# Kernel optimization log

Hardware: AMD Instinct MI355X
Metric: run time of the kernel (lower is better)

The kernel has to match this reference:

```python
import jax, jax.numpy as jnp
import numpy as np

C, H, W, D, M = 64, 512, 512, 4, 16


def setup_inputs() -> dict:
    key = jax.random.key(0)
    ks = jax.random.split(key, 9)
    scale = (1.0 / (C * C)) ** 0.5
    return {
        "q": jax.random.normal(ks[0], (1, 1, H, W), jnp.float32),
        "proj_w": jax.random.normal(ks[1], (C, 1, 1, 1), jnp.float32),
        "proj_b": jax.random.normal(ks[2], (C, 1, 1), jnp.float32) * 0.01,
        "spec_wr": jax.random.normal(ks[3], (D, C, C, M, M), jnp.float32) * scale,
        "spec_wi": jax.random.normal(ks[4], (D, C, C, M, M), jnp.float32) * scale,
        "w_w": jax.random.normal(ks[5], (D, C, C, 1, 1), jnp.float32) * (1.0 / C ** 0.5),
        "w_b": jax.random.normal(ks[6], (D, C, 1, 1), jnp.float32) * 0.01,
        "final_w": jax.random.normal(ks[7], (1, C, 1, 1), jnp.float32) * (1.0 / C ** 0.5),
        "final_b": jax.random.normal(ks[8], (1, 1, 1), jnp.float32) * 0.01,
    }


def _spectral(x, wr, wi, m):
    # x: (C,H,W). FFT2 -> contract low modes -> zero-pad -> iFFT2, take real part.
    Cin, Hh, Ww = x.shape
    x_ft = jnp.fft.fft2(x, axes=(-2, -1))  # (C,H,W) complex
    w = (wr + 1j * wi).astype(x_ft.dtype)  # (Cin,Cout,m,m)
    out_sub = jnp.einsum('imn,iomn->omn', x_ft[:, :m, :m], w)
    out_ft = jnp.zeros((wr.shape[1], Hh, Ww), dtype=x_ft.dtype).at[:, :m, :m].set(out_sub)
    return jnp.fft.ifft2(out_ft, axes=(-2, -1)).real


def reference(q, proj_w, proj_b, spec_wr, spec_wi, w_w, w_b, final_w, final_b):
    m = spec_wr.shape[-1]
    depth = spec_wr.shape[0]
    x = q[0].astype(jnp.float32)  # (C_in,H,W) -- batch must be 1
    # 1x1 conv lift
    x = jnp.einsum('oi,ihw->ohw', proj_w[:, :, 0, 0], x) + proj_b
    for d in range(depth):
        x_spec = _spectral(x, spec_wr[d], spec_wi[d], m)
        x_local = jnp.einsum('oi,ihw->ohw', w_w[d, :, :, 0, 0], x) + w_b[d]
        x = jax.nn.gelu(x_spec + x_local)
    x = jnp.einsum('oi,ihw->ohw', final_w[:, :, 0, 0], x) + final_b
    return x[None]  # re-add batch dim
```

## Files before the change

### kernel.cpp

```cpp
#include <hip/hip_runtime.h>
#include <cmath>

#define CC 64
#define HH 512
#define WWID 512
#define HWSZ (HH*WWID)
#define DEPTH 4

typedef __attribute__((ext_vector_type(8))) short short8;
typedef __attribute__((ext_vector_type(4))) float floatx4;

__device__ inline unsigned short f2bf(float f){
  unsigned int u = __float_as_uint(f);
  u += 0x7FFF + ((u >> 16) & 1);
  return (unsigned short)(u >> 16);
}
__device__ inline float bf2f(unsigned short h){
  return __uint_as_float(((unsigned int)h) << 16);
}

__global__ void k_init(const float* __restrict__ ww,
                       float* __restrict__ ctab, float* __restrict__ stab,
                       unsigned short* __restrict__ trigBh, unsigned short* __restrict__ trigBl,
                       unsigned short* __restrict__ trigTh, unsigned short* __restrict__ trigTl,
                       unsigned short* __restrict__ Whi, unsigned short* __restrict__ Wlo,
                       float4* __restrict__ Xfz){
  if (blockIdx.x < 32) Xfz[blockIdx.x*256 + threadIdx.x] = make_float4(0.f,0.f,0.f,0.f);
  int idx = blockIdx.x*256 + threadIdx.x;
  if (idx < 8192){
    int pos = idx >> 4, k = idx & 15;
    int r = (pos * k) & 511;
    double ang = (2.0 * 3.14159265358979323846 / 512.0) * (double)r;
    float c = (float)cos(ang), s = (float)sin(ang);
    ctab[idx] = c;  stab[idx] = s;
    unsigned short ch = f2bf(c), sh = f2bf(s);
    unsigned short cl = f2bf(c - bf2f(ch)), sl = f2bf(s - bf2f(sh));
    trigBh[pos*32 + 2*k]     = ch;  trigBl[pos*32 + 2*k]     = cl;
    trigBh[pos*32 + 2*k + 1] = sh;  trigBl[pos*32 + 2*k + 1] = sl;
    trigTh[(2*k)*512 + pos]   = ch;  trigTl[(2*k)*512 + pos]   = cl;
    trigTh[(2*k+1)*512 + pos] = sh;  trigTl[(2*k+1)*512 + pos] = sl;
  } else {
    int t = idx - 8192;
    float v = ww[t];
    unsigned short h = f2bf(v);
    Whi[t] = h;  Wlo[t] = f2bf(v - bf2f(h));
  }
}

#define APITCH 136
#define XPITCH 33
template<int LIFT>
__global__ __launch_bounds__(256) void k_dftw(const unsigned int* __restrict__ xp,
    const float* __restrict__ qsrc, const float* __restrict__ pw, const float* __restrict__ pb,
    const unsigned short* __restrict__ trigTh, const unsigned short* __restrict__ trigTl,
    const float* __restrict__ ctab, const float* __restrict__ stab,
    float* __restrict__ Xfa, float4* __restrict__ Yz){
  if (blockIdx.x < 32) Yz[blockIdx.x*256 + threadIdx.x] = make_float4(0.f,0.f,0.f,0.f);

  __shared__ unsigned short Ahs[64*APITCH], Als[64*APITCH];
  __shared__ unsigned short Bhs[32*APITCH], Bls[32*APITCH];
  __shared__ float X1s[64*XPITCH];
  int row0 = blockIdx.x * 64;
  int i  = row0 >> 9;
  int h0 = row0 & 511;
  int t = threadIdx.x;
  int g = t >> 6, lm = t & 15, lq = (t >> 4) & 3;
  float pa = 0.f, pbv = 0.f;
  if (LIFT){ pa = pw[i]; pbv = pb[i]; }

  floatx4 acc[2] = {{0.f,0.f,0.f,0.f},{0.f,0.f,0.f,0.f}};

  for (int kc = 0; kc < 4; ++kc){
    {
      int r = t >> 2, qq = t & 3;
      unsigned int* dh = (unsigned int*)&Ahs[r*APITCH + qq*32];
      unsigned int* dl = (unsigned int*)&Als[r*APITCH + qq*32];
      if (LIFT){
        const float4* src4 = (const float4*)(qsrc + (size_t)(h0 + r)*512 + kc*128 + qq*32);
        #pragma unroll
        for (int u = 0; u < 8; ++u){
          float4 v = src4[u];
          v.x = fmaf(pa, v.x, pbv); v.y = fmaf(pa, v.y, pbv);
          v.z = fmaf(pa, v.z, pbv); v.w = fmaf(pa, v.w, pbv);
          unsigned short h0_ = f2bf(v.x), h1 = f2bf(v.y), h2 = f2bf(v.z), h3 = f2bf(v.w);
          unsigned short g0 = f2bf(v.x - bf2f(h0_)), g1 = f2bf(v.y - bf2f(h1));
          unsigned short g2 = f2bf(v.z - bf2f(h2)), g3 = f2bf(v.w - bf2f(h3));
          uint2 ph, pl;
          ph.x = (unsigned)h0_ | ((unsigned)h1 << 16);
          ph.y = (unsigned)h2 | ((unsigned)h3 << 16);
          pl.x = (unsigned)g0 | ((unsigned)g1 << 16);
          pl.y = (unsigned)g2 | ((unsigned)g3 << 16);
          *(uint2*)&dh[u*2] = ph;
          *(uint2*)&dl[u*2] = pl;
        }
      } else {
        const uint4* srcp = (const uint4*)(xp + ((size_t)(h0 + r)*64 + i)*512 + kc*128 + qq*32);
        #pragma unroll
        for (int u = 0; u < 8; ++u){
          uint4 v = srcp[u];
          uint2 ph, pl;
          ph.x = (v.x & 0xffffu) | (v.y << 16);
          ph.y = (v.z & 0xffffu) | (v.w << 16);
          pl.x = (v.x >> 16) | (v.y & 0xffff0000u);
          pl.y = (v.z >> 16) | (v.w & 0xffff0000u);
          *(uint2*)&dh[u*2] = ph;
          *(uint2*)&dl[u*2] = pl;
        }
      }
    }
    {
      int j = t >> 3, qq = t & 7;
      const uint4* sh = (const uint4*)((const unsigned int*)trigTh + j*256 + kc*64 + qq*8);
      const uint4* sl = (const uint4*)((const unsigned int*)trigTl + j*256 + kc*64 + qq*8);
      uint4* dh = (uint4*)&Bhs[j*APITCH + qq*16];
      uint4* dl = (uint4*)&Bls[j*APITCH + qq*16];
      dh[0] = sh[0]; dh[1] = sh[1];
      dl[0] = sl[0]; dl[1] = sl[1];
    }
    __syncthreads();
    #pragma unroll
    for (int ks = 0; ks < 4; ++ks){
      short8 ah = *(const short8*)&Ahs[(g*16 + lm)*APITCH + ks*32 + lq*8];
      short8 al = *(const short8*)&Als[(g*16 + lm)*APITCH + ks*32 + lq*8];
      #pragma unroll
      for (int nt = 0; nt < 2; ++nt){
        short8 bh = *(const short8*)&Bhs[(nt*16 + lm)*APITCH + ks*32 + lq*8];
        short8 bl = *(const short8*)&Bls[(nt*16 + lm)*APITCH + ks*32 + lq*8];
        acc[nt] = __builtin_amdgcn_mfma_f32_16x16x32_bf16(ah, bh, acc[nt], 0, 0, 0);
        acc[nt] = __builtin_amdgcn_mfma_f32_16x16x32_bf16(ah, bl, acc[nt], 0, 0, 0);
        acc[nt] = __builtin_amdgcn_mfma_f32_16x16x32_bf16(al, bh, acc[nt], 0, 0, 0);
      }
    }
    __syncthreads();
  }
  #pragma unroll
  for (int nt = 0; nt < 2; ++nt){
    int j = nt*16 + lm;
    float sgn = (j & 1) ? -1.f : 1.f;
    #pragma unroll
    for (int rg = 0; rg < 4; ++rg){
      int m = g*16 + lq*4 + rg;
      X1s[m*XPITCH + j] = sgn * acc[nt][rg];
    }
  }
  __syncthreads();

  int mo = t >> 4, n = t & 15;
  float ar = 0.f, ai = 0.f;
  #pragma unroll 8
  for (int hh = 0; hh < 64; ++hh){
    int h = h0 + hh;
    float Re = X1s[hh*XPITCH + 2*n];
    float Im = X1s[hh*XPITCH + 2*n + 1];
    float c = ctab[h*16 + mo], s = stab[h*16 + mo];
    ar += Re*c + Im*s;
    ai += Im*c - Re*s;
  }
  atomicAdd(&Xfa[(i*256 + t)*2],     ar);
  atomicAdd(&Xfa[(i*256 + t)*2 + 1], ai);
}

__global__ void k_contract(const float2* __restrict__ Xf,
                           const float* __restrict__ wr, const float* __restrict__ wi,
                           float* __restrict__ Ya){
  int o = blockIdx.x, ic = blockIdx.y;
  int mn = blockIdx.z*64 + threadIdx.x;
  float ar = 0.f, ai = 0.f;
  int i0 = ic * 16;
  #pragma unroll
  for (int ii = 0; ii < 16; ++ii){
    int i = i0 + ii;
    float2 xf = Xf[i*256 + mn];
    float wrv = wr[(i*64 + o)*256 + mn];
    float wiv = wi[(i*64 + o)*256 + mn];
    ar += xf.x*wrv - xf.y*wiv;
    ai += xf.x*wiv + xf.y*wrv;
  }
  const float sc = 1.f/262144.f;
  atomicAdd(&Ya[(o*256 + mn)*2],     ar*sc);
  atomicAdd(&Ya[(o*256 + mn)*2 + 1], ai*sc);
}

__global__ void k_idfth(const float2* __restrict__ Y, const float* __restrict__ ct,
                        const float* __restrict__ st,
                        unsigned int* __restrict__ Thi, unsigned int* __restrict__ Tlo,
                        float4* __restrict__ Xfz){
  if (blockIdx.x < 32) Xfz[blockIdx.x*256 + threadIdx.x] = make_float4(0.f,0.f,0.f,0.f);
  int idx = blockIdx.x*256 + threadIdx.x;
  int n = idx & 15, o = (idx >> 4) & 63, h = idx >> 10;
  float ar = 0.f, ai = 0.f;
  #pragma unroll
  for (int m = 0; m < 16; ++m){
    float2 y = Y[(o<<8) + (m<<4) + n];
    float c = ct[h*16 + m], s = st[h*16 + m];
    ar += y.x*c - y.y*s;
    ai += y.x*s + y.y*c;
  }
  float tr = ar, ts = -ai;
  unsigned short rh = f2bf(tr), sh = f2bf(ts);
  Thi[idx] = (unsigned int)rh | ((unsigned int)sh << 16);
  unsigned short rl = f2bf(tr - bf2f(rh)), slr = f2bf(ts - bf2f(sh));
  Tlo[idx] = (unsigned int)rl | ((unsigned int)slr << 16);
}

#define PITCH 104
template<int LIFT, int FINAL>
__global__ __launch_bounds__(256) void k_combine(
    const unsigned int* __restrict__ xp, const float* __restrict__ qsrc,
    const float* __restrict__ pw, const float* __restrict__ pb,
    const unsigned short* __restrict__ Whid, const unsigned short* __restrict__ Wlod,
    const unsigned int* __restrict__ Thi,  const unsigned int* __restrict__ Tlo,
    const unsigned short* __restrict__ trigBh, const unsigned short* __restrict__ trigBl,
    const float* __restrict__ wb, unsigned int* __restrict__ xo,
    const float* __restrict__ fw, const float* __restrict__ fb,
    float* __restrict__ outp)
{
  __shared__ unsigned short Ah[64*PITCH],  Al[64*PITCH];
  __shared__ unsigned short Bh[128*PITCH], Bl[128*PITCH];
  int h  = blockIdx.y;
  int w0 = blockIdx.x * 128;
  int t  = threadIdx.x;

  {
    int wl = t & 127, ig = t >> 7;
    if (LIFT){
      float qv = qsrc[(size_t)h*512 + w0 + wl];
      #pragma unroll
      for (int ii = 0; ii < 32; ii += 4){
        int i0 = ig*32 + ii;
        float v0 = fmaf(pw[i0],   qv, pb[i0]);
        float v1 = fmaf(pw[i0+1], qv, pb[i0+1]);
        float v2 = fmaf(pw[i0+2], qv, pb[i0+2]);
        float v3 = fmaf(pw[i0+3], qv, pb[i0+3]);
        unsigned short h0 = f2bf(v0), h1 = f2bf(v1), h2 = f2bf(v2), h3 = f2bf(v3);
        unsigned short g0 = f2bf(v0 - bf2f(h0)), g1 = f2bf(v1 - bf2f(h1));
        unsigned short g2 = f2bf(v2 - bf2f(h2)), g3 = f2bf(v3 - bf2f(h3));
        uint2 ph, pl;
        ph.x = (unsigned)h0 | ((unsigned)h1 << 16);
        ph.y = (unsigned)h2 | ((unsigned)h3 << 16);
        pl.x = (unsigned)g0 | ((unsigned)g1 << 16);
        pl.y = (unsigned)g2 | ((unsigned)g3 << 16);
        *(uint2*)&Bh[wl*PITCH + i0] = ph;
        *(uint2*)&Bl[wl*PITCH + i0] = pl;
      }
    } else {
      const unsigned int* xb = xp + (size_t)h*32768 + w0 + wl;
      #pragma unroll
      for (int ii = 0; ii < 32; ii += 4){
        int i0 = ig*32 + ii;
        unsigned int v0 = xb[(size_t)(i0  )*512];
        unsigned int v1 = xb[(size_t)(i0+1)*512];
        unsigned int v2 = xb[(size_t)(i0+2)*512];
        unsigned int v3 = xb[(size_t)(i0+3)*512];
        uint2 ph, pl;
        ph.x = (v0 & 0xffffu) | (v1 << 16);
        ph.y = (v2 & 0xffffu) | (v3 << 16);
        pl.x = (v0 >> 16) | (v1 & 0xffff0000u);
        pl.y = (v2 >> 16) | (v3 & 0xffff0000u);
        *(uint2*)&Bh[wl*PITCH + i0] = ph;
        *(uint2*)&Bl[wl*PITCH + i0] = pl;
      }
    }
  }
  {
    int row = t >> 1, qq = t & 1;
    const uint4* sh = (const uint4*)((const unsigned int*)trigBh + (size_t)(w0+row)*16 + qq*8);
    const uint4* sl = (const uint4*)((const unsigned int*)trigBl + (size_t)(w0+row)*16 + qq*8);
    uint4* dh = (uint4*)((unsigned int*)&Bh[row*PITCH + 64] + qq*8);
    uint4* dl = (uint4*)((unsigned int*)&Bl[row*PITCH + 64] + qq*8);
    dh[0] = sh[0]; dh[1] = sh[1];
    dl[0] = sl[0]; dl[1] = sl[1];
  }
  {
    int o = t >> 2, q8 = t & 3;
    const uint4* sh = (const uint4*)((const unsigned int*)Whid + o*32 + q8*8);
    const uint4* sl = (const uint4*)((const unsigned int*)Wlod + o*32 + q8*8);
    uint4* dh = (uint4*)((unsigned int*)&Ah[o*PITCH] + q8*8);
    uint4* dl = (uint4*)((unsigned int*)&Al[o*PITCH] + q8*8);
    dh[0] = sh[0]; dh[1] = sh[1];
    dl[0] = sl[0]; dl[1] = sl[1];
  }
  {
    int o = t >> 2, q4 = t & 3;
    const uint4* sh = (const uint4*)(Thi + (size_t)h*1024 + o*16 + q4*4);
    const uint4* sl = (const uint4*)(Tlo + (size_t)h*1024 + o*16 + q4*4);
    uint4* dh = (uint4*)((unsigned int*)&Ah[o*PITCH + 64] + q4*4);
    uint4* dl = (uint4*)((unsigned int*)&Al[o*PITCH + 64] + q4*4);
    dh[0] = sh[0];
    dl[0] = sl[0];
  }
  __syncthreads();

  int g  = t >> 6;
  int lm = t & 15;
  int lq = (t >> 4) & 3;

  floatx4 acc[8] = {{0.f,0.f,0.f,0.f},{0.f,0.f,0.f,0.f},{0.f,0.f,0.f,0.f},{0.f,0.f,0.f,0.f},
                    {0.f,0.f,0.f,0.f},{0.f,0.f,0.f,0.f},{0.f,0.f,0.f,0.f},{0.f,0.f,0.f,0.f}};

  #pragma unroll
  for (int ks = 0; ks < 3; ++ks){
    short8 af = *(const short8*)&Ah[(g*16 + lm)*PITCH + ks*32 + lq*8];
    short8 al = *(const short8*)&Al[(g*16 + lm)*PITCH + ks*32 + lq*8];
    #pragma unroll
    for (int nt = 0; nt < 8; ++nt){
      short8 bf = *(const short8*)&Bh[(nt*16 + lm)*PITCH + ks*32 + lq*8];
      short8 bl = *(const short8*)&Bl[(nt*16 + lm)*PITCH + ks*32 + lq*8];
      acc[nt] = __builtin_amdgcn_mfma_f32_16x16x32_bf16(af, bf, acc[nt], 0, 0, 0);
      acc[nt] = __builtin_amdgcn_mfma_f32_16x16x32_bf16(af, bl, acc[nt], 0, 0, 0);
      acc[nt] = __builtin_amdgcn_mfma_f32_16x16x32_bf16(al, bf, acc[nt], 0, 0, 0);
    }
  }

  if (!FINAL){
    #pragma unroll
    for (int nt = 0; nt < 8; ++nt){
      int w = w0 + nt*16 + lm;
      #pragma unroll
      for (int rg = 0; rg < 4; ++rg){
        int o = g*16 + lq*4 + rg;
        float u = acc[nt][rg] + wb[o];
        float z = 0.7978845608028654f * fmaf(0.044715f, u*u*u, u);
        float e = __expf(2.f*z);
        float gl = u - __fdividef(u, e + 1.f);
        unsigned short hi_ = f2bf(gl);
        unsigned short lo_ = f2bf(gl - bf2f(hi_));
        xo[((size_t)h*64 + o)*512 + w] = (unsigned int)hi_ | ((unsigned int)lo_ << 16);
      }
    }
  } else {
    float* fred = (float*)Ah;
    __syncthreads();
    #pragma unroll
    for (int nt = 0; nt < 8; ++nt){
      float partial = 0.f;
      #pragma unroll
      for (int rg = 0; rg < 4; ++rg){
        int o = g*16 + lq*4 + rg;
        float u = acc[nt][rg] + wb[o];
        float z = 0.7978845608028654f * fmaf(0.044715f, u*u*u, u);
        float e = __expf(2.f*z);
        float gl = u - __fdividef(u, e + 1.f);
        partial = fmaf(fw[o], gl, partial);
      }
      fred[(nt*16 + lm)*17 + (t >> 4)] = partial;
    }
    __syncthreads();
    if (t < 128){
      float s = fb[0];
      #pragma unroll
      for (int k2 = 0; k2 < 16; ++k2) s += fred[t*17 + k2];
      outp[(size_t)h*512 + w0 + t] = s;
    }
  }
}

extern "C" void kernel_launch(void* const* d_in, const int* in_sizes, int n_in,
                              void* d_out, int out_size, void* d_ws, size_t ws_size,
                              hipStream_t stream) {
  const float* q       = (const float*)d_in[0];
  const float* proj_w  = (const float*)d_in[1];
  const float* proj_b  = (const float*)d_in[2];
  const float* spec_wr = (const float*)d_in[3];
  const float* spec_wi = (const float*)d_in[4];
  const float* w_w     = (const float*)d_in[5];
  const float* w_b     = (const float*)d_in[6];
  const float* final_w = (const float*)d_in[7];
  const float* final_b = (const float*)d_in[8];
  float* out = (float*)d_out;

  char* ws = (char*)d_ws;
  float*  ctab = (float*) (ws + 0);
  float*  stab = (float*) (ws + 32768);
  unsigned short* trigBh = (unsigned short*)(ws + 65536);
  unsigned short* trigBl = (unsigned short*)(ws + 98304);
  unsigned int* Thi = (unsigned int*)(ws + 131072);
  unsigned int* Tlo = (unsigned int*)(ws + 2228224);
  float*  Xf   = (float*) (ws + 4325376);
  float*  Y    = (float*) (ws + 4456448);
  unsigned int* x = (unsigned int*)(ws + 4587520);
  unsigned short* Whi = (unsigned short*)(ws + 71696384);
  unsigned short* Wlo = (unsigned short*)(ws + 71729152);
  unsigned short* trigTh = (unsigned short*)(ws + 71761920);
  unsigned short* trigTl = (unsigned short*)(ws + 71794688);

  k_init<<<96, 256, 0, stream>>>(w_w, ctab, stab, trigBh, trigBl, trigTh, trigTl,
                                 Whi, Wlo, (float4*)Xf);

  for (int d = 0; d < DEPTH; ++d){
    if (d == 0)
      k_dftw<1><<<512, 256, 0, stream>>>(x, q, proj_w, proj_b, trigTh, trigTl,
                                         ctab, stab, Xf, (float4*)Y);
    else
      k_dftw<0><<<512, 256, 0, stream>>>(x, q, proj_w, proj_b, trigTh, trigTl,
                                         ctab, stab, Xf, (float4*)Y);
    k_contract<<<dim3(64,4,4), 64, 0, stream>>>((const float2*)Xf,
                                                spec_wr + (size_t)d*1048576,
                                                spec_wi + (size_t)d*1048576, Y);
    k_idfth<<<2048, 256, 0, stream>>>((const float2*)Y, ctab, stab, Thi, Tlo,
                                      (float4*)Xf);
    if (d == 0)
      k_combine<1,0><<<dim3(4,512), 256, 0, stream>>>(x, q, proj_w, proj_b,
          Whi + d*4096, Wlo + d*4096, Thi, Tlo, trigBh, trigBl,
          w_b + d*64, x, final_w, final_b, out);
    else if (d < DEPTH-1)
      k_combine<0,0><<<dim3(4,512), 256, 0, stream>>>(x, q, proj_w, proj_b,
          Whi + d*4096, Wlo + d*4096, Thi, Tlo, trigBh, trigBl,
          w_b + d*64, x, final_w, final_b, out);
    else
      k_combine<0,1><<<dim3(4,512), 256, 0, stream>>>(x, q, proj_w, proj_b,
          Whi + d*4096, Wlo + d*4096, Thi, Tlo, trigBh, trigBl,
          w_b + d*64, x, final_w, final_b, out);
  }
}
```

Before: 326.5 us.

## Load combine-kernel B operands directly from global into registers, dropping LDS staging

```diff
diff --git a/kernel.cpp b/kernel.cpp
--- a/kernel.cpp
+++ b/kernel.cpp
@@ -205,7 +205,7 @@
 
 #define PITCH 104
 template<int LIFT, int FINAL>
-__global__ __launch_bounds__(256) void k_combine(
+__global__ __launch_bounds__(256, 4) void k_combine(
     const unsigned int* __restrict__ xp, const float* __restrict__ qsrc,
     const float* __restrict__ pw, const float* __restrict__ pb,
     const unsigned short* __restrict__ Whid, const unsigned short* __restrict__ Wlod,
@@ -215,62 +215,11 @@
     const float* __restrict__ fw, const float* __restrict__ fb,
     float* __restrict__ outp)
 {
-  __shared__ unsigned short Ah[64*PITCH],  Al[64*PITCH];
-  __shared__ unsigned short Bh[128*PITCH], Bl[128*PITCH];
+  __shared__ unsigned short Ah[64*PITCH], Al[64*PITCH];
   int h  = blockIdx.y;
   int w0 = blockIdx.x * 128;
   int t  = threadIdx.x;
 
-  {
-    int wl = t & 127, ig = t >> 7;
-    if (LIFT){
-      float qv = qsrc[(size_t)h*512 + w0 + wl];
-      #pragma unroll
-      for (int ii = 0; ii < 32; ii += 4){
-        int i0 = ig*32 + ii;
-        float v0 = fmaf(pw[i0],   qv, pb[i0]);
-        float v1 = fmaf(pw[i0+1], qv, pb[i0+1]);
-        float v2 = fmaf(pw[i0+2], qv, pb[i0+2]);
-        float v3 = fmaf(pw[i0+3], qv, pb[i0+3]);
-        unsigned short h0 = f2bf(v0), h1 = f2bf(v1), h2 = f2bf(v2), h3 = f2bf(v3);
-        unsigned short g0 = f2bf(v0 - bf2f(h0)), g1 = f2bf(v1 - bf2f(h1));
-        unsigned short g2 = f2bf(v2 - bf2f(h2)), g3 = f2bf(v3 - bf2f(h3));
-        uint2 ph, pl;
-        ph.x = (unsigned)h0 | ((unsigned)h1 << 16);
-        ph.y = (unsigned)h2 | ((unsigned)h3 << 16);
-        pl.x = (unsigned)g0 | ((unsigned)g1 << 16);
-        pl.y = (unsigned)g2 | ((unsigned)g3 << 16);
-        *(uint2*)&Bh[wl*PITCH + i0] = ph;
-        *(uint2*)&Bl[wl*PITCH + i0] = pl;
-      }
-    } else {
-      const unsigned int* xb = xp + (size_t)h*32768 + w0 + wl;
-      #pragma unroll
-      for (int ii = 0; ii < 32; ii += 4){
-        int i0 = ig*32 + ii;
-        unsigned int v0 = xb[(size_t)(i0  )*512];
-        unsigned int v1 = xb[(size_t)(i0+1)*512];
-        unsigned int v2 = xb[(size_t)(i0+2)*512];
-        unsigned int v3 = xb[(size_t)(i0+3)*512];
-        uint2 ph, pl;
-        ph.x = (v0 & 0xffffu) | (v1 << 16);
-        ph.y = (v2 & 0xffffu) | (v3 << 16);
-        pl.x = (v0 >> 16) | (v1 & 0xffff0000u);
-        pl.y = (v2 >> 16) | (v3 & 0xffff0000u);
-        *(uint2*)&Bh[wl*PITCH + i0] = ph;
-        *(uint2*)&Bl[wl*PITCH + i0] = pl;
-      }
-    }
-  }
-  {
-    int row = t >> 1, qq = t & 1;
-    const uint4* sh = (const uint4*)((const unsigned int*)trigBh + (size_t)(w0+row)*16 + qq*8);
-    const uint4* sl = (const uint4*)((const unsigned int*)trigBl + (size_t)(w0+row)*16 + qq*8);
-    uint4* dh = (uint4*)((unsigned int*)&Bh[row*PITCH + 64] + qq*8);
-    uint4* dl = (uint4*)((unsigned int*)&Bl[row*PITCH + 64] + qq*8);
-    dh[0] = sh[0]; dh[1] = sh[1];
-    dl[0] = sl[0]; dl[1] = sl[1];
-  }
   {
     int o = t >> 2, q8 = t & 3;
     const uint4* sh = (const uint4*)((const unsigned int*)Whid + o*32 + q8*8);
@@ -295,21 +244,70 @@
   int lm = t & 15;
   int lq = (t >> 4) & 3;
 
+  short8 af0 = *(const short8*)&Ah[(g*16 + lm)*PITCH +  0 + lq*8];
+  short8 al0 = *(const short8*)&Al[(g*16 + lm)*PITCH +  0 + lq*8];
+  short8 af1 = *(const short8*)&Ah[(g*16 + lm)*PITCH + 32 + lq*8];
+  short8 al1 = *(const short8*)&Al[(g*16 + lm)*PITCH + 32 + lq*8];
+  short8 af2 = *(const short8*)&Ah[(g*16 + lm)*PITCH + 64 + lq*8];
+  short8 al2 = *(const short8*)&Al[(g*16 + lm)*PITCH + 64 + lq*8];
+
   floatx4 acc[8] = {{0.f,0.f,0.f,0.f},{0.f,0.f,0.f,0.f},{0.f,0.f,0.f,0.f},{0.f,0.f,0.f,0.f},
                     {0.f,0.f,0.f,0.f},{0.f,0.f,0.f,0.f},{0.f,0.f,0.f,0.f},{0.f,0.f,0.f,0.f}};
 
+  const unsigned int* xw = xp + (size_t)h*32768;
+  float pwv[16], pbv[16];
+  if (LIFT){
+    #pragma unroll
+    for (int u = 0; u < 8; ++u){
+      pwv[u]   = pw[lq*8 + u];      pbv[u]   = pb[lq*8 + u];
+      pwv[8+u] = pw[32 + lq*8 + u]; pbv[8+u] = pb[32 + lq*8 + u];
+    }
+  }
+
   #pragma unroll
-  for (int ks = 0; ks < 3; ++ks){
-    short8 af = *(const short8*)&Ah[(g*16 + lm)*PITCH + ks*32 + lq*8];
-    short8 al = *(const short8*)&Al[(g*16 + lm)*PITCH + ks*32 + lq*8];
-    #pragma unroll
-    for (int nt = 0; nt < 8; ++nt){
-      short8 bf = *(const short8*)&Bh[(nt*16 + lm)*PITCH + ks*32 + lq*8];
-      short8 bl = *(const short8*)&Bl[(nt*16 + lm)*PITCH + ks*32 + lq*8];
-      acc[nt] = __builtin_amdgcn_mfma_f32_16x16x32_bf16(af, bf, acc[nt], 0, 0, 0);
-      acc[nt] = __builtin_amdgcn_mfma_f32_16x16x32_bf16(af, bl, acc[nt], 0, 0, 0);
-      acc[nt] = __builtin_amdgcn_mfma_f32_16x16x32_bf16(al, bf, acc[nt], 0, 0, 0);
-    }
+  for (int nt = 0; nt < 8; ++nt){
+    int w = w0 + nt*16 + lm;
+    unsigned int v0[8], v1[8];
+    if (LIFT){
+      float qv = qsrc[(size_t)h*512 + w];
+      #pragma unroll
+      for (int u = 0; u < 8; ++u){
+        float a = fmaf(pwv[u], qv, pbv[u]);
+        unsigned short hh = f2bf(a), ll = f2bf(a - bf2f(hh));
+        v0[u] = (unsigned int)hh | ((unsigned int)ll << 16);
+        float b = fmaf(pwv[8+u], qv, pbv[8+u]);
+        unsigned short hb = f2bf(b), lb = f2bf(b - bf2f(hb));
+        v1[u] = (unsigned int)hb | ((unsigned int)lb << 16);
+      }
+    } else {
+      #pragma unroll
+      for (int u = 0; u < 8; ++u){
+        v0[u] = xw[(size_t)(     lq*8 + u)*512 + w];
+        v1[u] = xw[(size_t)(32 + lq*8 + u)*512 + w];
+      }
+    }
+    unsigned int f0[4], l0[4], f1[4], l1[4];
+    #pragma unroll
+    for (int p = 0; p < 4; ++p){
+      f0[p] = (v0[2*p] & 0xffffu) | (v0[2*p+1] << 16);
+      l0[p] = (v0[2*p] >> 16)     | (v0[2*p+1] & 0xffff0000u);
+      f1[p] = (v1[2*p] & 0xffffu) | (v1[2*p+1] << 16);
+      l1[p] = (v1[2*p] >> 16)     | (v1[2*p+1] & 0xffff0000u);
+    }
+    short8 bf0 = *(short8*)f0, bl0 = *(short8*)l0;
+    short8 bf1 = *(short8*)f1, bl1 = *(short8*)l1;
+    short8 bf2 = *(const short8*)(trigBh + (size_t)w*32 + lq*8);
+    short8 bl2 = *(const short8*)(trigBl + (size_t)w*32 + lq*8);
+
+    acc[nt] = __builtin_amdgcn_mfma_f32_16x16x32_bf16(af0, bf0, acc[nt], 0, 0, 0);
+    acc[nt] = __builtin_amdgcn_mfma_f32_16x16x32_bf16(af0, bl0, acc[nt], 0, 0, 0);
+    acc[nt] = __builtin_amdgcn_mfma_f32_16x16x32_bf16(al0, bf0, acc[nt], 0, 0, 0);
+    acc[nt] = __builtin_amdgcn_mfma_f32_16x16x32_bf16(af1, bf1, acc[nt], 0, 0, 0);
+    acc[nt] = __builtin_amdgcn_mfma_f32_16x16x32_bf16(af1, bl1, acc[nt], 0, 0, 0);
+    acc[nt] = __builtin_amdgcn_mfma_f32_16x16x32_bf16(al1, bf1, acc[nt], 0, 0, 0);
+    acc[nt] = __builtin_amdgcn_mfma_f32_16x16x32_bf16(af2, bf2, acc[nt], 0, 0, 0);
+    acc[nt] = __builtin_amdgcn_mfma_f32_16x16x32_bf16(af2, bl2, acc[nt], 0, 0, 0);
+    acc[nt] = __builtin_amdgcn_mfma_f32_16x16x32_bf16(al2, bf2, acc[nt], 0, 0, 0);
   }
 
   if (!FINAL){
```

New measurement: 338.7 us. 3.7% more time.
